# Optimization experiments

Hardware: AMD Instinct MI355X
Metric: run time of the kernel (lower is better)

The kernel has to match this reference:

```python
import jax, jax.numpy as jnp
import numpy as np

B, H, S, D = 2, 8, 2048, 64
ALPHA = 1
P_NORM = 2
EPS = 1e-5


def setup_inputs() -> dict:
    key = jax.random.key(0)
    kq, kk, kv = jax.random.split(key, 3)
    query = jax.random.normal(kq, (B, H, S, D), dtype=jnp.float32)
    keys = jax.random.normal(kk, (B, H, S, D), dtype=jnp.float32)
    vals = jax.random.normal(kv, (B, H, S, D), dtype=jnp.float32)
    # causal mask: 1 where attention allowed, 0 elsewhere (masked_fill on mask==0)
    mask = jnp.tril(jnp.ones((S, S), dtype=jnp.int32))[None, None, :, :]
    return {"query": query, "keys": keys, "vals": vals, "mask": mask}


def reference(query, keys, vals, mask):
    d = query.shape[-1]
    sqrt_d = jnp.asarray(d, query.dtype) ** 0.5
    # L2-normalized cosine similarity term
    q_n = query / jnp.linalg.norm(query, axis=-1, keepdims=True)
    k_n = keys / jnp.linalg.norm(keys, axis=-1, keepdims=True)
    cos = jnp.einsum('bhqd,bhkd->bhqk', q_n, k_n)
    rq = (1.0 + (1.0 - cos) / (ALPHA * sqrt_d)) ** (-ALPHA)
    preattn = jnp.log(rq + EPS)
    # magnitude term: (||q||_p^p + ||k||_p^p) / (2 sqrt(d))
    q_mag = jnp.sum(jnp.abs(query) ** P_NORM, axis=-1, keepdims=True)  # [B,H,S,1]
    k_mag = jnp.sum(jnp.abs(keys) ** P_NORM, axis=-1, keepdims=True)   # [B,H,S,1]
    preattn = preattn + (q_mag + jnp.swapaxes(k_mag, -2, -1)) / (2.0 * sqrt_d)
    preattn = jnp.where(mask == 0, -jnp.inf, preattn)
    attn = jax.nn.softmax(preattn, axis=-1)
    out = jnp.einsum('bhqk,bhkd->bhqd', attn, vals)
    return out, attn
```

## Files before the change

kernel.cpp:

```cpp
#include <hip/hip_runtime.h>
#include <math.h>


#define BH 16
#define SS 2048
#define DD 64
#define NKT 32

typedef float f4a __attribute__((ext_vector_type(4)));
typedef short bs8 __attribute__((ext_vector_type(8)));
typedef short bs4 __attribute__((ext_vector_type(4)));
typedef unsigned int u32x2 __attribute__((ext_vector_type(2)));

__device__ __forceinline__ short bf16rne(float f) {
  unsigned u = __float_as_uint(f);
  u += 0x7fffu + ((u >> 16) & 1u);
  return (short)(u >> 16);
}
__device__ __forceinline__ float truncb(float x) {
  return __uint_as_float(__float_as_uint(x) & 0xffff0000u);
}
__device__ __forceinline__ unsigned packhi(float lo, float hi) {
  return (__float_as_uint(hi) & 0xffff0000u) | (__float_as_uint(lo) >> 16);
}

__device__ __forceinline__ f4a mfma16(bs4 a, bs4 b, f4a c) {
#if __has_builtin(__builtin_amdgcn_mfma_f32_16x16x16bf16_1k)
  return __builtin_amdgcn_mfma_f32_16x16x16bf16_1k(a, b, c, 0, 0, 0);
#else
  f4a d;
  asm("v_mfma_f32_16x16x16_bf16 %0, %1, %2, %3"
      : "=v"(d)
      : "v"(a), "v"(b), "v"(c));
  return d;
#endif
}

__global__ __launch_bounds__(256) void rq_rowss(const float* __restrict__ q,
                                                const float* __restrict__ k,
                                                float* __restrict__ ws) {
  int gid = blockIdx.x * 256 + threadIdx.x;
  int grp = gid >> 4;
  int lane = gid & 15;
  const int nrows = BH * SS;
  const float* src = (grp < nrows) ? q : k;
  int row = (grp < nrows) ? grp : (grp - nrows);
  float4 v = *(const float4*)(src + (size_t)row * DD + lane * 4);
  float s = v.x * v.x + v.y * v.y + v.z * v.z + v.w * v.w;
  s += __shfl_xor(s, 1);
  s += __shfl_xor(s, 2);
  s += __shfl_xor(s, 4);
  s += __shfl_xor(s, 8);
  if (lane == 0) ws[grp] = s;
}

__global__ __launch_bounds__(256, 3) void rq_attn(const float* __restrict__ Q,
                                                  const float* __restrict__ K,
                                                  const float* __restrict__ V,
                                                  const float* __restrict__ ss,
                                                  float* __restrict__ outp,
                                                  float* __restrict__ attnp) {
  __shared__ short smemS[12288];
  __shared__ float ektS[64];
  __shared__ float lrowp[2][64];
  __shared__ float lrow[64];
  short* const Kf = smemS;
  short* const VtH = smemS + 4096;
  short* const VtL = smemS + 8192;

  const int t = threadIdx.x;
  const int bx = blockIdx.x;
  const int qt = NKT - 1 - (bx >> 4);
  const int bh = bx & 15;
  const int qbase = qt * 64;
  const float* Qg = Q + (size_t)bh * SS * DD;
  const float* Kg = K + (size_t)bh * SS * DD;
  const float* Vg = V + (size_t)bh * SS * DD;
  float* Ag = attnp + (size_t)bh * SS * SS;
  const float* qss = ss + (size_t)bh * SS;
  const float* kss = ss + (size_t)(BH * SS) + (size_t)bh * SS;

  const int l = t & 63;
  const int wv = t >> 6;
  const int qrh = wv >> 1;
  const int kch = wv & 1;
  const int l15 = l & 15;
  const int lh = l >> 4;

  const int ukb = ((((l15 >> 2) & 3) | (((lh >> 1) & 1) << 2) |
                    ((lh & 1) << 3) | ((l15 & 3) << 4)) << 3);

  const int s_rb = (t >> 4) << 2;
  const int s_c0 = (t & 15) << 2;
  const int kw_ks = s_c0 >> 5;
  const int kw_dgrp = (s_c0 >> 3) & 3;
  const int kw_e0 = s_c0 & 7;
  const int kw_ub = (((t >> 4) & 3) | (((kw_dgrp >> 1) & 1) << 2) |
                     ((kw_dgrp & 1) << 3) | (((t >> 4) >> 2) << 6));

  auto stageK = [&](int kbase) {
#pragma unroll
    for (int i = 0; i < 4; ++i) {
      const int kc = s_rb + i;
      float4 v = *(const float4*)(Kg + (size_t)(kbase + kc) * DD + s_c0);
      float rn = rsqrtf(kss[kbase + kc]);
      bs4 b;
      b[0] = bf16rne(v.x * rn);
      b[1] = bf16rne(v.y * rn);
      b[2] = bf16rne(v.z * rn);
      b[3] = bf16rne(v.w * rn);
      *(bs4*)&Kf[kw_ks * 2048 + (kw_ub | (i << 4)) * 8 + kw_e0] = b;
    }
    if (t < 64) ektS[t] = __expf(kss[kbase + t] * 0.0625f);
  };

  auto stageV = [&](int kbase) {
    float mm[4][4];
#pragma unroll
    for (int i = 0; i < 4; ++i)
      *(float4*)&mm[i][0] =
          *(const float4*)(Vg + (size_t)(kbase + s_rb + i) * DD + s_c0);
    const int kgw = t >> 4;
#pragma unroll
    for (int j = 0; j < 4; ++j) {
      const int d = s_c0 + j;
      const int si = (d * 16 + (kgw ^ (d & 15))) * 4;
      u32x2 h, lo2;
      h.x = packhi(mm[0][j], mm[1][j]);
      h.y = packhi(mm[2][j], mm[3][j]);
      float r0 = mm[0][j] - truncb(mm[0][j]);
      float r1 = mm[1][j] - truncb(mm[1][j]);
      float r2 = mm[2][j] - truncb(mm[2][j]);
      float r3 = mm[3][j] - truncb(mm[3][j]);
      lo2.x = packhi(r0, r1);
      lo2.y = packhi(r2, r3);
      *(u32x2*)&VtH[si] = h;
      *(u32x2*)&VtL[si] = lo2;
    }
  };

  bs8 qf[2][2];
#pragma unroll
  for (int mb = 0; mb < 2; ++mb) {
    const int row = qbase + qrh * 32 + mb * 16 + l15;
    const float rn = rsqrtf(qss[row]);
#pragma unroll
    for (int ks = 0; ks < 2; ++ks) {
      const float* src = Qg + (size_t)row * DD + ks * 32 + lh * 8;
      float4 x = *(const float4*)src;
      float4 y = *(const float4*)(src + 4);
      bs8 q;
      q[0] = bf16rne(x.x * rn);
      q[1] = bf16rne(x.y * rn);
      q[2] = bf16rne(x.z * rn);
      q[3] = bf16rne(x.w * rn);
      q[4] = bf16rne(y.x * rn);
      q[5] = bf16rne(y.y * rn);
      q[6] = bf16rne(y.z * rn);
      q[7] = bf16rne(y.w * rn);
      qf[mb][ks] = q;
    }
  }

  const f4a fz = {0.f, 0.f, 0.f, 0.f};

  float rs0 = 0.f, rs1 = 0.f;
  for (int kt = 0; kt <= qt; ++kt) {
    const int kbase = kt * 64;
    stageK(kbase);
    __syncthreads();

    f4a acc[4];
    acc[0] = fz; acc[1] = fz; acc[2] = fz; acc[3] = fz;
#pragma unroll
    for (int ks = 0; ks < 2; ++ks)
#pragma unroll
      for (int nb = 0; nb < 2; ++nb) {
        bs8 kf = *(const bs8*)&Kf[ks * 2048 + ((kch * 2 + nb) << 9) + ukb];
#pragma unroll
        for (int mb = 0; mb < 2; ++mb)
          acc[mb * 2 + nb] = __builtin_amdgcn_mfma_f32_16x16x32_bf16(
              kf, qf[mb][ks], acc[mb * 2 + nb], 0, 0, 0);
      }

    const bool diag = (kt == qt);
#pragma unroll
    for (int nb = 0; nb < 2; ++nb) {
      float ekr[4];
#pragma unroll
      for (int r = 0; r < 4; ++r)
        ekr[r] = ektS[kch * 32 + nb * 16 + lh * 4 + r];
#pragma unroll
      for (int mb = 0; mb < 2; ++mb) {
        const int qg = qrh * 32 + mb * 16 + l15;
#pragma unroll
        for (int r = 0; r < 4; ++r) {
          const int kg = kch * 32 + nb * 16 + lh * 4 + r;
          float w = fmaf(8.0f,
                         __builtin_amdgcn_rcpf(9.0f - acc[mb * 2 + nb][r]),
                         1e-5f) * ekr[r];
          if (diag && kg > qg) w = 0.0f;
          if (mb) rs1 += w; else rs0 += w;
        }
      }
    }
    __syncthreads();
  }

  rs0 += __shfl_xor(rs0, 16);
  rs0 += __shfl_xor(rs0, 32);
  rs1 += __shfl_xor(rs1, 16);
  rs1 += __shfl_xor(rs1, 32);
  if (l < 16) {
    lrowp[kch][qrh * 32 + l15] = rs0;
    lrowp[kch][qrh * 32 + 16 + l15] = rs1;
  }
  __syncthreads();
  if (t < 64) lrow[t] = 1.0f / (lrowp[0][t] + lrowp[1][t]);
  __syncthreads();
  const float li0 = lrow[qrh * 32 + l15];
  const float li1 = lrow[qrh * 32 + 16 + l15];

  f4a O[8];
#pragma unroll
  for (int i = 0; i < 8; ++i) O[i] = fz;

  for (int kt = 0; kt <= qt; ++kt) {
    const int kbase = kt * 64;
    stageK(kbase);
    stageV(kbase);
    __syncthreads();

    f4a acc[4];
    acc[0] = fz; acc[1] = fz; acc[2] = fz; acc[3] = fz;
#pragma unroll
    for (int ks = 0; ks < 2; ++ks)
#pragma unroll
      for (int nb = 0; nb < 2; ++nb) {
        bs8 kf = *(const bs8*)&Kf[ks * 2048 + ((kch * 2 + nb) << 9) + ukb];
#pragma unroll
        for (int mb = 0; mb < 2; ++mb)
          acc[mb * 2 + nb] = __builtin_amdgcn_mfma_f32_16x16x32_bf16(
              kf, qf[mb][ks], acc[mb * 2 + nb], 0, 0, 0);
      }

    u32x2 pH[2][2], pL[2][2];
    const bool diag = (kt == qt);
#pragma unroll
    for (int nb = 0; nb < 2; ++nb) {
      float ekr[4];
#pragma unroll
      for (int r = 0; r < 4; ++r)
        ekr[r] = ektS[kch * 32 + nb * 16 + lh * 4 + r];
#pragma unroll
      for (int mb = 0; mb < 2; ++mb) {
        const int qg = qrh * 32 + mb * 16 + l15;
        const float li = mb ? li1 : li0;
        float av[4];
#pragma unroll
        for (int r = 0; r < 4; ++r) {
          const int kg = kch * 32 + nb * 16 + lh * 4 + r;
          float w = fmaf(8.0f,
                         __builtin_amdgcn_rcpf(9.0f - acc[mb * 2 + nb][r]),
                         1e-5f) * ekr[r];
          if (diag && kg > qg) w = 0.0f;
          av[r] = w * li;
        }
        f4a a4 = {av[0], av[1], av[2], av[3]};
        __builtin_nontemporal_store(
            a4, (f4a*)(Ag + (size_t)(qbase + qg) * SS + kbase + kch * 32 +
                       nb * 16 + lh * 4));
        pH[mb][nb].x = packhi(av[0], av[1]);
        pH[mb][nb].y = packhi(av[2], av[3]);
        float r0 = av[0] - truncb(av[0]);
        float r1 = av[1] - truncb(av[1]);
        float r2 = av[2] - truncb(av[2]);
        float r3 = av[3] - truncb(av[3]);
        pL[mb][nb].x = packhi(r0, r1);
        pL[mb][nb].y = packhi(r2, r3);
      }
    }

#pragma unroll
    for (int nb = 0; nb < 2; ++nb) {
      const int kg = kch * 8 + nb * 4 + lh;
#pragma unroll
      for (int db = 0; db < 4; ++db) {
        const int d = db * 16 + l15;
        const int si = (d * 16 + (kg ^ (d & 15))) * 4;
        bs4 VH = *(const bs4*)&VtH[si];
        bs4 VL = *(const bs4*)&VtL[si];
#pragma unroll
        for (int mb = 0; mb < 2; ++mb) {
          bs4 AH = __builtin_bit_cast(bs4, pH[mb][nb]);
          bs4 AL = __builtin_bit_cast(bs4, pL[mb][nb]);
          O[mb * 4 + db] = mfma16(AH, VH, O[mb * 4 + db]);
          O[mb * 4 + db] = mfma16(AH, VL, O[mb * 4 + db]);
          O[mb * 4 + db] = mfma16(AL, VH, O[mb * 4 + db]);
        }
      }
    }
    __syncthreads();
  }

  {
    const f4a z = {0.f, 0.f, 0.f, 0.f};
    const int r0i = (t >> 4) << 2;
    const int c0i = (t & 15) << 2;
    for (int kt = qt + 1; kt < NKT; ++kt) {
#pragma unroll
      for (int i = 0; i < 4; ++i)
        __builtin_nontemporal_store(
            z, (f4a*)(Ag + (size_t)(qbase + r0i + i) * SS + kt * 64 + c0i));
    }
  }

  float* Osc = (float*)smemS;
  if (kch == 1) {
#pragma unroll
    for (int mb = 0; mb < 2; ++mb)
#pragma unroll
      for (int db = 0; db < 4; ++db)
#pragma unroll
        for (int r = 0; r < 4; ++r)
          Osc[(qrh * 32 + mb * 16 + lh * 4 + r) * 64 + db * 16 + l15] =
              O[mb * 4 + db][r];
  }
  __syncthreads();
  if (kch == 0) {
    float* Og = outp + (size_t)bh * SS * DD;
#pragma unroll
    for (int mb = 0; mb < 2; ++mb)
#pragma unroll
      for (int db = 0; db < 4; ++db)
#pragma unroll
        for (int r = 0; r < 4; ++r) {
          const int row = qrh * 32 + mb * 16 + lh * 4 + r;
          Og[(size_t)(qbase + row) * DD + db * 16 + l15] =
              O[mb * 4 + db][r] + Osc[row * 64 + db * 16 + l15];
        }
  }
}

extern "C" void kernel_launch(void* const* d_in, const int* in_sizes, int n_in,
                              void* d_out, int out_size, void* d_ws, size_t ws_size,
                              hipStream_t stream) {
  const float* q = (const float*)d_in[0];
  const float* k = (const float*)d_in[1];
  const float* v = (const float*)d_in[2];
  float* out = (float*)d_out;
  float* attn = out + (size_t)BH * SS * DD;
  float* ws = (float*)d_ws;

  rq_rowss<<<dim3((2 * BH * SS) / 16), dim3(256), 0, stream>>>(q, k, ws);
  rq_attn<<<dim3(NKT * 16), dim3(256), 0, stream>>>(q, k, v, ws, out, attn);
}
```

Measured before the change: 399.1 us.

## Double block to 512 threads, one 16-row query tile per wave, split staging

Each block now has 8 waves instead of 4, and each wave handles a single 16-row query slice instead of two. In the second pass, half the threads stage V while the other half stage K. This raises waves per CU and spreads staging across more threads, at the cost of less reuse of each K fragment read from LDS per MFMA. The PV MFMAs are reordered so all V fragments are loaded before the MFMA chains.

```diff
diff --git a/kernel.cpp b/kernel.cpp
--- a/kernel.cpp
+++ b/kernel.cpp
@@ -34,6 +34,11 @@
       : "v"(a), "v"(b), "v"(c));
   return d;
 #endif
+}
+
+__device__ __forceinline__ int kunit(int kc, int dgrp) {
+  return ((kc >> 2) & 3) | (((dgrp >> 1) & 1) << 2) | ((dgrp & 1) << 3) |
+         ((kc & 3) << 4) | ((kc >> 4) << 6);
 }
 
 __global__ __launch_bounds__(256) void rq_rowss(const float* __restrict__ q,
@@ -54,7 +59,7 @@
   if (lane == 0) ws[grp] = s;
 }
 
-__global__ __launch_bounds__(256, 3) void rq_attn(const float* __restrict__ Q,
+__global__ __launch_bounds__(512, 4) void rq_attn(const float* __restrict__ Q,
                                                   const float* __restrict__ K,
                                                   const float* __restrict__ V,
                                                   const float* __restrict__ ss,
@@ -81,68 +86,43 @@
   const float* kss = ss + (size_t)(BH * SS) + (size_t)bh * SS;
 
   const int l = t & 63;
-  const int wv = t >> 6;
-  const int qrh = wv >> 1;
-  const int kch = wv & 1;
+  const int wid = t >> 6;
+  const int qq = wid >> 1;
+  const int kch = wid & 1;
   const int l15 = l & 15;
   const int lh = l >> 4;
 
-  const int ukb = ((((l15 >> 2) & 3) | (((lh >> 1) & 1) << 2) |
-                    ((lh & 1) << 3) | ((l15 & 3) << 4)) << 3);
-
-  const int s_rb = (t >> 4) << 2;
+  const int ukb = kunit(l15, lh) * 8;
+
+  const int p1_kc = t >> 3;
+  const int p1_df = t & 7;
+  const int p1_ks = p1_df >> 2;
+  const int p1_addr = p1_ks * 2048 + kunit(p1_kc, p1_df & 3) * 8;
+
+  auto stageK_unit = [&](int kbase, int kc, int df, int addr) {
+    const float* src = Kg + (size_t)(kbase + kc) * DD + df * 8;
+    float4 x = *(const float4*)src;
+    float4 y = *(const float4*)(src + 4);
+    float rn = rsqrtf(kss[kbase + kc]);
+    bs8 b;
+    b[0] = bf16rne(x.x * rn);
+    b[1] = bf16rne(x.y * rn);
+    b[2] = bf16rne(x.z * rn);
+    b[3] = bf16rne(x.w * rn);
+    b[4] = bf16rne(y.x * rn);
+    b[5] = bf16rne(y.y * rn);
+    b[6] = bf16rne(y.z * rn);
+    b[7] = bf16rne(y.w * rn);
+    *(bs8*)&Kf[addr] = b;
+  };
+
+  const int s_rb = ((t & 255) >> 4) << 2;
   const int s_c0 = (t & 15) << 2;
-  const int kw_ks = s_c0 >> 5;
-  const int kw_dgrp = (s_c0 >> 3) & 3;
-  const int kw_e0 = s_c0 & 7;
-  const int kw_ub = (((t >> 4) & 3) | (((kw_dgrp >> 1) & 1) << 2) |
-                     ((kw_dgrp & 1) << 3) | (((t >> 4) >> 2) << 6));
-
-  auto stageK = [&](int kbase) {
-#pragma unroll
-    for (int i = 0; i < 4; ++i) {
-      const int kc = s_rb + i;
-      float4 v = *(const float4*)(Kg + (size_t)(kbase + kc) * DD + s_c0);
-      float rn = rsqrtf(kss[kbase + kc]);
-      bs4 b;
-      b[0] = bf16rne(v.x * rn);
-      b[1] = bf16rne(v.y * rn);
-      b[2] = bf16rne(v.z * rn);
-      b[3] = bf16rne(v.w * rn);
-      *(bs4*)&Kf[kw_ks * 2048 + (kw_ub | (i << 4)) * 8 + kw_e0] = b;
-    }
-    if (t < 64) ektS[t] = __expf(kss[kbase + t] * 0.0625f);
-  };
-
-  auto stageV = [&](int kbase) {
-    float mm[4][4];
-#pragma unroll
-    for (int i = 0; i < 4; ++i)
-      *(float4*)&mm[i][0] =
-          *(const float4*)(Vg + (size_t)(kbase + s_rb + i) * DD + s_c0);
-    const int kgw = t >> 4;
-#pragma unroll
-    for (int j = 0; j < 4; ++j) {
-      const int d = s_c0 + j;
-      const int si = (d * 16 + (kgw ^ (d & 15))) * 4;
-      u32x2 h, lo2;
-      h.x = packhi(mm[0][j], mm[1][j]);
-      h.y = packhi(mm[2][j], mm[3][j]);
-      float r0 = mm[0][j] - truncb(mm[0][j]);
-      float r1 = mm[1][j] - truncb(mm[1][j]);
-      float r2 = mm[2][j] - truncb(mm[2][j]);
-      float r3 = mm[3][j] - truncb(mm[3][j]);
-      lo2.x = packhi(r0, r1);
-      lo2.y = packhi(r2, r3);
-      *(u32x2*)&VtH[si] = h;
-      *(u32x2*)&VtL[si] = lo2;
-    }
-  };
-
-  bs8 qf[2][2];
-#pragma unroll
-  for (int mb = 0; mb < 2; ++mb) {
-    const int row = qbase + qrh * 32 + mb * 16 + l15;
+  const int kgw = (t & 255) >> 4;
+
+  bs8 qf[2];
+  {
+    const int row = qbase + qq * 16 + l15;
     const float rn = rsqrtf(qss[row]);
 #pragma unroll
     for (int ks = 0; ks < 2; ++ks) {
@@ -158,158 +138,165 @@
       q[5] = bf16rne(y.y * rn);
       q[6] = bf16rne(y.z * rn);
       q[7] = bf16rne(y.w * rn);
-      qf[mb][ks] = q;
+      qf[ks] = q;
     }
   }
 
   const f4a fz = {0.f, 0.f, 0.f, 0.f};
 
-  float rs0 = 0.f, rs1 = 0.f;
+  float rs = 0.f;
   for (int kt = 0; kt <= qt; ++kt) {
     const int kbase = kt * 64;
-    stageK(kbase);
+    stageK_unit(kbase, p1_kc, p1_df, p1_addr);
+    if (t < 64) ektS[t] = __expf(kss[kbase + t] * 0.0625f);
     __syncthreads();
 
-    f4a acc[4];
-    acc[0] = fz; acc[1] = fz; acc[2] = fz; acc[3] = fz;
+    f4a acc[2];
+    acc[0] = fz;
+    acc[1] = fz;
 #pragma unroll
     for (int ks = 0; ks < 2; ++ks)
 #pragma unroll
       for (int nb = 0; nb < 2; ++nb) {
         bs8 kf = *(const bs8*)&Kf[ks * 2048 + ((kch * 2 + nb) << 9) + ukb];
-#pragma unroll
-        for (int mb = 0; mb < 2; ++mb)
-          acc[mb * 2 + nb] = __builtin_amdgcn_mfma_f32_16x16x32_bf16(
-              kf, qf[mb][ks], acc[mb * 2 + nb], 0, 0, 0);
+        acc[nb] = __builtin_amdgcn_mfma_f32_16x16x32_bf16(kf, qf[ks], acc[nb],
+                                                          0, 0, 0);
       }
 
     const bool diag = (kt == qt);
-#pragma unroll
-    for (int nb = 0; nb < 2; ++nb) {
-      float ekr[4];
-#pragma unroll
-      for (int r = 0; r < 4; ++r)
-        ekr[r] = ektS[kch * 32 + nb * 16 + lh * 4 + r];
-#pragma unroll
-      for (int mb = 0; mb < 2; ++mb) {
-        const int qg = qrh * 32 + mb * 16 + l15;
-#pragma unroll
-        for (int r = 0; r < 4; ++r) {
-          const int kg = kch * 32 + nb * 16 + lh * 4 + r;
-          float w = fmaf(8.0f,
-                         __builtin_amdgcn_rcpf(9.0f - acc[mb * 2 + nb][r]),
-                         1e-5f) * ekr[r];
-          if (diag && kg > qg) w = 0.0f;
-          if (mb) rs1 += w; else rs0 += w;
-        }
-      }
-    }
+    const int qg = qq * 16 + l15;
+#pragma unroll
+    for (int nb = 0; nb < 2; ++nb)
+#pragma unroll
+      for (int r = 0; r < 4; ++r) {
+        const int kg = kch * 32 + nb * 16 + lh * 4 + r;
+        float w = fmaf(8.0f, __builtin_amdgcn_rcpf(9.0f - acc[nb][r]), 1e-5f) *
+                  ektS[kg];
+        if (diag && kg > qg) w = 0.0f;
+        rs += w;
+      }
     __syncthreads();
   }
 
-  rs0 += __shfl_xor(rs0, 16);
-  rs0 += __shfl_xor(rs0, 32);
-  rs1 += __shfl_xor(rs1, 16);
-  rs1 += __shfl_xor(rs1, 32);
-  if (l < 16) {
-    lrowp[kch][qrh * 32 + l15] = rs0;
-    lrowp[kch][qrh * 32 + 16 + l15] = rs1;
-  }
+  rs += __shfl_xor(rs, 16);
+  rs += __shfl_xor(rs, 32);
+  if (l < 16) lrowp[kch][qq * 16 + l15] = rs;
   __syncthreads();
   if (t < 64) lrow[t] = 1.0f / (lrowp[0][t] + lrowp[1][t]);
   __syncthreads();
-  const float li0 = lrow[qrh * 32 + l15];
-  const float li1 = lrow[qrh * 32 + 16 + l15];
-
-  f4a O[8];
-#pragma unroll
-  for (int i = 0; i < 8; ++i) O[i] = fz;
+  const float li = lrow[qq * 16 + l15];
+
+  f4a O[4];
+#pragma unroll
+  for (int i = 0; i < 4; ++i) O[i] = fz;
 
   for (int kt = 0; kt <= qt; ++kt) {
     const int kbase = kt * 64;
-    stageK(kbase);
-    stageV(kbase);
+    if (t < 256) {
+      float mm[4][4];
+#pragma unroll
+      for (int i = 0; i < 4; ++i)
+        *(float4*)&mm[i][0] =
+            *(const float4*)(Vg + (size_t)(kbase + s_rb + i) * DD + s_c0);
+#pragma unroll
+      for (int j = 0; j < 4; ++j) {
+        const int d = s_c0 + j;
+        const int si = (d * 16 + (kgw ^ (d & 15))) * 4;
+        u32x2 h, lo2;
+        h.x = packhi(mm[0][j], mm[1][j]);
+        h.y = packhi(mm[2][j], mm[3][j]);
+        float r0 = mm[0][j] - truncb(mm[0][j]);
+        float r1 = mm[1][j] - truncb(mm[1][j]);
+        float r2 = mm[2][j] - truncb(mm[2][j]);
+        float r3 = mm[3][j] - truncb(mm[3][j]);
+        lo2.x = packhi(r0, r1);
+        lo2.y = packhi(r2, r3);
+        *(u32x2*)&VtH[si] = h;
+        *(u32x2*)&VtL[si] = lo2;
+      }
+      if (t < 64) ektS[t] = __expf(kss[kbase + t] * 0.0625f);
+    } else {
+      const int tp = t - 256;
+      const int kc = tp >> 2;
+      const int df0 = (tp & 3) << 1;
+#pragma unroll
+      for (int u = 0; u < 2; ++u) {
+        const int df = df0 + u;
+        stageK_unit(kbase, kc, df, (df >> 2) * 2048 + kunit(kc, df & 3) * 8);
+      }
+    }
     __syncthreads();
 
-    f4a acc[4];
-    acc[0] = fz; acc[1] = fz; acc[2] = fz; acc[3] = fz;
+    f4a acc[2];
+    acc[0] = fz;
+    acc[1] = fz;
 #pragma unroll
     for (int ks = 0; ks < 2; ++ks)
 #pragma unroll
       for (int nb = 0; nb < 2; ++nb) {
         bs8 kf = *(const bs8*)&Kf[ks * 2048 + ((kch * 2 + nb) << 9) + ukb];
-#pragma unroll
-        for (int mb = 0; mb < 2; ++mb)
-          acc[mb * 2 + nb] = __builtin_amdgcn_mfma_f32_16x16x32_bf16(
-              kf, qf[mb][ks], acc[mb * 2 + nb], 0, 0, 0);
-      }
-
-    u32x2 pH[2][2], pL[2][2];
+        acc[nb] = __builtin_amdgcn_mfma_f32_16x16x32_bf16(kf, qf[ks], acc[nb],
+                                                          0, 0, 0);
+      }
+
+    u32x2 pH[2], pL[2];
     const bool diag = (kt == qt);
+    const int qg = qq * 16 + l15;
 #pragma unroll
     for (int nb = 0; nb < 2; ++nb) {
-      float ekr[4];
-#pragma unroll
-      for (int r = 0; r < 4; ++r)
-        ekr[r] = ektS[kch * 32 + nb * 16 + lh * 4 + r];
-#pragma unroll
-      for (int mb = 0; mb < 2; ++mb) {
-        const int qg = qrh * 32 + mb * 16 + l15;
-        const float li = mb ? li1 : li0;
-        float av[4];
-#pragma unroll
-        for (int r = 0; r < 4; ++r) {
-          const int kg = kch * 32 + nb * 16 + lh * 4 + r;
-          float w = fmaf(8.0f,
-                         __builtin_amdgcn_rcpf(9.0f - acc[mb * 2 + nb][r]),
-                         1e-5f) * ekr[r];
-          if (diag && kg > qg) w = 0.0f;
-          av[r] = w * li;
-        }
-        f4a a4 = {av[0], av[1], av[2], av[3]};
-        __builtin_nontemporal_store(
-            a4, (f4a*)(Ag + (size_t)(qbase + qg) * SS + kbase + kch * 32 +
-                       nb * 16 + lh * 4));
-        pH[mb][nb].x = packhi(av[0], av[1]);
-        pH[mb][nb].y = packhi(av[2], av[3]);
-        float r0 = av[0] - truncb(av[0]);
-        float r1 = av[1] - truncb(av[1]);
-        float r2 = av[2] - truncb(av[2]);
-        float r3 = av[3] - truncb(av[3]);
-        pL[mb][nb].x = packhi(r0, r1);
-        pL[mb][nb].y = packhi(r2, r3);
-      }
+      float av[4];
+#pragma unroll
+      for (int r = 0; r < 4; ++r) {
+        const int kg = kch * 32 + nb * 16 + lh * 4 + r;
+        float w = fmaf(8.0f, __builtin_amdgcn_rcpf(9.0f - acc[nb][r]), 1e-5f) *
+                  ektS[kg];
+        if (diag && kg > qg) w = 0.0f;
+        av[r] = w * li;
+      }
+      f4a a4 = {av[0], av[1], av[2], av[3]};
+      __builtin_nontemporal_store(
+          a4, (f4a*)(Ag + (size_t)(qbase + qg) * SS + kbase + kch * 32 +
+                     nb * 16 + lh * 4));
+      pH[nb].x = packhi(av[0], av[1]);
+      pH[nb].y = packhi(av[2], av[3]);
+      float r0 = av[0] - truncb(av[0]);
+      float r1 = av[1] - truncb(av[1]);
+      float r2 = av[2] - truncb(av[2]);
+      float r3 = av[3] - truncb(av[3]);
+      pL[nb].x = packhi(r0, r1);
+      pL[nb].y = packhi(r2, r3);
     }
 
 #pragma unroll
     for (int nb = 0; nb < 2; ++nb) {
       const int kg = kch * 8 + nb * 4 + lh;
+      bs4 VH[4], VL[4];
 #pragma unroll
       for (int db = 0; db < 4; ++db) {
         const int d = db * 16 + l15;
         const int si = (d * 16 + (kg ^ (d & 15))) * 4;
-        bs4 VH = *(const bs4*)&VtH[si];
-        bs4 VL = *(const bs4*)&VtL[si];
-#pragma unroll
-        for (int mb = 0; mb < 2; ++mb) {
-          bs4 AH = __builtin_bit_cast(bs4, pH[mb][nb]);
-          bs4 AL = __builtin_bit_cast(bs4, pL[mb][nb]);
-          O[mb * 4 + db] = mfma16(AH, VH, O[mb * 4 + db]);
-          O[mb * 4 + db] = mfma16(AH, VL, O[mb * 4 + db]);
-          O[mb * 4 + db] = mfma16(AL, VH, O[mb * 4 + db]);
-        }
-      }
+        VH[db] = *(const bs4*)&VtH[si];
+        VL[db] = *(const bs4*)&VtL[si];
+      }
+      const bs4 AH = __builtin_bit_cast(bs4, pH[nb]);
+      const bs4 AL = __builtin_bit_cast(bs4, pL[nb]);
+#pragma unroll
+      for (int db = 0; db < 4; ++db) O[db] = mfma16(AH, VH[db], O[db]);
+#pragma unroll
+      for (int db = 0; db < 4; ++db) O[db] = mfma16(AH, VL[db], O[db]);
+#pragma unroll
+      for (int db = 0; db < 4; ++db) O[db] = mfma16(AL, VH[db], O[db]);
     }
     __syncthreads();
   }
 
   {
     const f4a z = {0.f, 0.f, 0.f, 0.f};
-    const int r0i = (t >> 4) << 2;
+    const int r0i = (t >> 4) << 1;
     const int c0i = (t & 15) << 2;
     for (int kt = qt + 1; kt < NKT; ++kt) {
 #pragma unroll
-      for (int i = 0; i < 4; ++i)
+      for (int i = 0; i < 2; ++i)
         __builtin_nontemporal_store(
             z, (f4a*)(Ag + (size_t)(qbase + r0i + i) * SS + kt * 64 + c0i));
     }
@@ -318,27 +305,22 @@
   float* Osc = (float*)smemS;
   if (kch == 1) {
 #pragma unroll
-    for (int mb = 0; mb < 2; ++mb)
-#pragma unroll
-      for (int db = 0; db < 4; ++db)
-#pragma unroll
-        for (int r = 0; r < 4; ++r)
-          Osc[(qrh * 32 + mb * 16 + lh * 4 + r) * 64 + db * 16 + l15] =
-              O[mb * 4 + db][r];
+    for (int db = 0; db < 4; ++db)
+#pragma unroll
+      for (int r = 0; r < 4; ++r)
+        Osc[(qq * 16 + lh * 4 + r) * 64 + db * 16 + l15] = O[db][r];
   }
   __syncthreads();
   if (kch == 0) {
     float* Og = outp + (size_t)bh * SS * DD;
 #pragma unroll
-    for (int mb = 0; mb < 2; ++mb)
-#pragma unroll
-      for (int db = 0; db < 4; ++db)
-#pragma unroll
-        for (int r = 0; r < 4; ++r) {
-          const int row = qrh * 32 + mb * 16 + lh * 4 + r;
-          Og[(size_t)(qbase + row) * DD + db * 16 + l15] =
-              O[mb * 4 + db][r] + Osc[row * 64 + db * 16 + l15];
-        }
+    for (int db = 0; db < 4; ++db)
+#pragma unroll
+      for (int r = 0; r < 4; ++r) {
+        const int row = qq * 16 + lh * 4 + r;
+        Og[(size_t)(qbase + row) * DD + db * 16 + l15] =
+            O[db][r] + Osc[row * 64 + db * 16 + l15];
+      }
   }
 }
 
@@ -353,5 +335,5 @@
   float* ws = (float*)d_ws;
 
   rq_rowss<<<dim3((2 * BH * SS) / 16), dim3(256), 0, stream>>>(q, k, ws);
-  rq_attn<<<dim3(NKT * 16), dim3(256), 0, stream>>>(q, k, v, ws, out, attn);
-}
+  rq_attn<<<dim3(NKT * 16), dim3(512), 0, stream>>>(q, k, v, ws, out, attn);
+}
```

New measurement: 401.8 us. About the same (+0.7%).
